# Performance work log

Measured on AMD Instinct MI355X. Metric: run time of the kernel, lower is better.

## Reference

```python
import jax, jax.numpy as jnp
import numpy as np

B, S, D, H = 2, 2048, 1024, 16
HD = D // H  # head depth


def setup_inputs() -> dict:
    key = jax.random.key(0)
    ks = jax.random.split(key, 8)
    scale = 0.02
    K = jax.random.normal(ks[0], (B, S, D), jnp.float32)
    V = jax.random.normal(ks[1], (B, S, D), jnp.float32)
    Q = jax.random.normal(ks[2], (B, S, D), jnp.float32)
    # causal additive mask: 1.0 where attention is disallowed (strict upper triangle)
    mask = jnp.broadcast_to(
        jnp.triu(jnp.ones((S, S), jnp.float32), k=1)[None, None, :, :], (B, 1, S, S)
    )
    Wk = jax.random.normal(ks[3], (D, D), jnp.float32) * scale
    Wv = jax.random.normal(ks[4], (D, D), jnp.float32) * scale
    Wq = jax.random.normal(ks[5], (D, D), jnp.float32) * scale
    Wo = jax.random.normal(ks[6], (D, D), jnp.float32) * scale
    z = jnp.zeros((D,), jnp.float32)
    return {"K": K, "V": V, "Q": Q, "mask": mask,
            "Wk": Wk, "bk": z, "Wv": Wv, "bv": z,
            "Wq": Wq, "bq": z, "Wo": Wo, "bo": z}


def _split_heads(x):  # [B,S,D] -> [B,H,S,HD]
    return x.reshape(B, S, H, HD).transpose(0, 2, 1, 3)


def reference(K, V, Q, mask, Wk, bk, Wv, bv, Wq, bq, Wo, bo):
    k = _split_heads(K @ Wk + bk)
    v = _split_heads(V @ Wv + bv)
    q = _split_heads(Q @ Wq + bq)
    # NOTE: source scales by sqrt(d_model), not sqrt(head_depth)
    logits = jnp.einsum("bhqd,bhkd->bhqk", q, k) / jnp.sqrt(jnp.float32(D))
    logits = logits + mask * (-1e9)
    attn = jax.nn.softmax(logits, axis=-1)
    out = jnp.einsum("bhqk,bhkd->bhqd", attn, v)  # [B,H,S,HD]
    out = out.transpose(0, 2, 1, 3).reshape(B, S, D)
    return out @ Wo + bo
```

## Files before the change

### kernel.cpp

```cpp
#include <hip/hip_runtime.h>
#include <hip/hip_bf16.h>

typedef unsigned short u16;
typedef unsigned int u32;
typedef unsigned long long u64;
typedef __attribute__((ext_vector_type(8))) __bf16 bf16x8;
typedef __attribute__((ext_vector_type(4))) float f32x4;

#define SEQ 2048
#define DM 1024
#define NH 16
#define HDim 64

__device__ __forceinline__ float bf_lo(u32 u) { return __uint_as_float(u << 16); }
__device__ __forceinline__ float bf_hi(u32 u) { return __uint_as_float(u & 0xffff0000u); }
__device__ __forceinline__ u16 f2bf(float f) {
    u32 u = __float_as_uint(f);
    u32 r = (u + 0x7fffu + ((u >> 16) & 1u)) >> 16;
    return (u16)r;
}
__device__ __forceinline__ float bf2f(u16 h) { return __uint_as_float(((u32)h) << 16); }

#define GLD16(g, l)                                                         \
    __builtin_amdgcn_global_load_lds(                                       \
        (const __attribute__((address_space(1))) void*)(g),                 \
        (__attribute__((address_space(3))) void*)(l), 16, 0, 0)

__device__ __forceinline__ bool detect_f32(const u32* q)
{
    const u32 w = q[threadIdx.x & 63];
    const int e0 = ((w & 0xffffu) >> 7) & 0xff;
    const int e1 = (w >> 23) & 0xff;
    const unsigned long long b = __ballot(e0 >= 0x90 || e1 >= 0x90);
    return b != 0ull;
}

__global__ __launch_bounds__(256)
void prep_all(const void* __restrict__ Qin, const void* __restrict__ Kin,
              const void* __restrict__ Vin,
              const void* __restrict__ w0, const void* __restrict__ w1,
              const void* __restrict__ w2, const void* __restrict__ w3,
              const void* __restrict__ b0, const void* __restrict__ b1,
              const void* __restrict__ b2, const void* __restrict__ b3,
              u16* __restrict__ Xall, u16* __restrict__ Wtall,
              u16* __restrict__ ball)
{
    __shared__ u16 T[64 * 66];
    const bool f = detect_f32((const u32*)Qin);
    const int t = threadIdx.x;
    const int bid = blockIdx.x;

    if (bid < 6144) {
        const int z = bid >> 11;
        const int bx = bid & 2047;
        const void* src = (z == 0) ? Qin : (z == 1) ? Kin : Vin;
        const size_t i0 = ((size_t)bx * 256 + t) * 8;
        u16* d = Xall + (size_t)z * 4194304 + i0;
        if (f) {
            const uint4* s = reinterpret_cast<const uint4*>((const float*)src + i0);
            uint4 a = s[0], b = s[1];
            u16 o[8];
            o[0] = f2bf(__uint_as_float(a.x)); o[1] = f2bf(__uint_as_float(a.y));
            o[2] = f2bf(__uint_as_float(a.z)); o[3] = f2bf(__uint_as_float(a.w));
            o[4] = f2bf(__uint_as_float(b.x)); o[5] = f2bf(__uint_as_float(b.y));
            o[6] = f2bf(__uint_as_float(b.z)); o[7] = f2bf(__uint_as_float(b.w));
            *reinterpret_cast<uint4*>(d) = *reinterpret_cast<const uint4*>(o);
        } else {
            *reinterpret_cast<uint4*>(d) =
                *reinterpret_cast<const uint4*>((const u16*)src + i0);
        }
    } else if (bid < 7168) {
        const int r = bid - 6144;
        const int z = r >> 8;
        const void* src = (z == 0) ? w0 : (z == 1) ? w1 : (z == 2) ? w2 : w3;
        const int n0 = ((r >> 4) & 15) * 64;
        const int k0 = (r & 15) * 64;
        const int c = t & 63, g = t >> 6;
        if (f) {
            const float* W = (const float*)src;
#pragma unroll
            for (int i = 0; i < 16; i++) {
                const int kl = g * 16 + i;
                T[kl * 66 + c] = f2bf(W[(size_t)(k0 + kl) * DM + n0 + c]);
            }
        } else {
            const u16* W = (const u16*)src;
#pragma unroll
            for (int i = 0; i < 16; i++) {
                const int kl = g * 16 + i;
                T[kl * 66 + c] = W[(size_t)(k0 + kl) * DM + n0 + c];
            }
        }
        __syncthreads();
        u16* dst = Wtall + (size_t)z * 1048576;
#pragma unroll
        for (int i = 0; i < 16; i++) {
            const int nl = g * 16 + i;
            dst[(size_t)(n0 + nl) * DM + k0 + c] = T[c * 66 + nl];
        }
    } else {
#pragma unroll
        for (int j = 0; j < 16; j++) {
            const int idx = t * 16 + j;
            const int z = idx >> 10, e = idx & 1023;
            const void* src = (z == 0) ? b0 : (z == 1) ? b1 : (z == 2) ? b2 : b3;
            ball[idx] = f ? f2bf(((const float*)src)[e]) : ((const u16*)src)[e];
        }
    }
}

__global__ __launch_bounds__(256)
void gemm128(const u16* __restrict__ Xall, const u16* __restrict__ Wtall,
             const u16* __restrict__ ball, u16* __restrict__ Yall)
{
    __shared__ __align__(16) u16 As[2][128 * 32];
    __shared__ __align__(16) u16 Bs[2][128 * 32];

    const int zz = blockIdx.z;
    const bool swp = (zz != 2);
    const u16* X  = Xall + (size_t)zz * 4194304;
    const u16* Wt = Wtall + (size_t)zz * 1048576;

    const int t    = threadIdx.x;
    const int w    = t >> 6;
    const int lane = t & 63;
    const int quad = lane >> 4;
    const int ln   = lane & 15;
    const int m0   = blockIdx.x * 128;
    const int n0   = blockIdx.y * 128;

    f32x4 acc[4][4];
#pragma unroll
    for (int i = 0; i < 4; i++)
#pragma unroll
        for (int j = 0; j < 4; j++) acc[i][j] = (f32x4){0.f, 0.f, 0.f, 0.f};

    const int swz = (lane >> 3) & 3;
    const u16* ag = X  + (size_t)(m0 + w * 32 + (lane >> 2)) * DM + ((lane & 3) ^ swz) * 8;
    const u16* bg = Wt + (size_t)(n0 + w * 32 + (lane >> 2)) * DM + ((lane & 3) ^ swz) * 8;

    const int wr = (w >> 1) * 64;
    const int wc = (w & 1) * 64;
    const int rs = (quad ^ ((ln >> 1) & 3)) * 8;

#define GSTAGE(B)                                        \
    {                                                    \
        GLD16(ag,           &As[B][w * 1024]);           \
        GLD16(ag + 16 * DM, &As[B][w * 1024 + 512]);     \
        GLD16(bg,           &Bs[B][w * 1024]);           \
        GLD16(bg + 16 * DM, &Bs[B][w * 1024 + 512]);     \
        ag += 32; bg += 32;                              \
    }

#define GCOMP(B)                                                              \
    {                                                                         \
        bf16x8 af[4], bfr[4];                                                 \
        _Pragma("unroll") for (int rt = 0; rt < 4; rt++)                      \
            af[rt] = *reinterpret_cast<const bf16x8*>(                        \
                &As[B][(wr + rt * 16 + ln) * 32 + rs]);                       \
        _Pragma("unroll") for (int ct = 0; ct < 4; ct++)                      \
            bfr[ct] = *reinterpret_cast<const bf16x8*>(                       \
                &Bs[B][(wc + ct * 16 + ln) * 32 + rs]);                       \
        if (swp) {                                                            \
            _Pragma("unroll") for (int rt = 0; rt < 4; rt++)                  \
                _Pragma("unroll") for (int ct = 0; ct < 4; ct++)              \
                    acc[rt][ct] = __builtin_amdgcn_mfma_f32_16x16x32_bf16(    \
                        bfr[ct], af[rt], acc[rt][ct], 0, 0, 0);               \
        } else {                                                              \
            _Pragma("unroll") for (int rt = 0; rt < 4; rt++)                  \
                _Pragma("unroll") for (int ct = 0; ct < 4; ct++)              \
                    acc[rt][ct] = __builtin_amdgcn_mfma_f32_16x16x32_bf16(    \
                        af[rt], bfr[ct], acc[rt][ct], 0, 0, 0);               \
        }                                                                     \
    }

    GSTAGE(0);
    __syncthreads();
#pragma unroll 1
    for (int it = 0; it < 15; ++it) {
        GSTAGE(1); GCOMP(0); __syncthreads();
        GSTAGE(0); GCOMP(1); __syncthreads();
    }
    GSTAGE(1); GCOMP(0); __syncthreads();
    GCOMP(1);
#undef GSTAGE
#undef GCOMP

    u16* Y = Yall + (size_t)zz * 4194304;

    if (swp) {
        const float scale = (zz == 0) ? 0.03125f : 1.0f;
#pragma unroll
        for (int ct = 0; ct < 4; ct++) {
            const int nb = n0 + wc + ct * 16 + quad * 4;
            const int h = nb >> 6, hd = nb & (HDim - 1);
            float bv[4];
#pragma unroll
            for (int r = 0; r < 4; r++) bv[r] = bf2f(ball[zz * 1024 + nb + r]);
#pragma unroll
            for (int rt = 0; rt < 4; rt++) {
                const int m = m0 + wr + rt * 16 + ln;
                const int b = m >> 11, s = m & (SEQ - 1);
                u16 o4[4];
#pragma unroll
                for (int r = 0; r < 4; r++)
                    o4[r] = f2bf((acc[rt][ct][r] + bv[r]) * scale);
                *reinterpret_cast<u64*>(
                    Y + (((size_t)(b * NH + h)) * SEQ + s) * HDim + hd) =
                    *reinterpret_cast<const u64*>(o4);
            }
        }
    } else {
#pragma unroll
        for (int ct = 0; ct < 4; ct++) {
            const int n = n0 + wc + ct * 16 + ln;
            const float bv = bf2f(ball[zz * 1024 + n]);
            const int h = n >> 6, hd = n & (HDim - 1);
#pragma unroll
            for (int rt = 0; rt < 4; rt++) {
                const int m = m0 + wr + rt * 16 + quad * 4;
                const int b = m >> 11, s = m & (SEQ - 1);
                u16 o4[4];
#pragma unroll
                for (int r = 0; r < 4; r++) o4[r] = f2bf(acc[rt][ct][r] + bv);
                *reinterpret_cast<u64*>(
                    Y + (((size_t)(b * NH + h) * HDim + hd) * SEQ + s)) =
                    *reinterpret_cast<const u64*>(o4);
            }
        }
    }
}

__device__ __forceinline__ void attn_tile2(
    const u16* __restrict__ Ks, const u16* __restrict__ Vs,
    u16* __restrict__ Ps, const bf16x8& qf0, const bf16x8& qf1,
    int kt, int qrow, int w, int quad, int ln, f32x4* o, float& l)
{
    f32x4 s[4];
#pragma unroll
    for (int ct = 0; ct < 4; ct++) {
        const u16* kr = &Ks[(ct * 16 + ln) * 72 + quad * 8];
        bf16x8 kf0 = *reinterpret_cast<const bf16x8*>(kr);
        bf16x8 kf1 = *reinterpret_cast<const bf16x8*>(kr + 32);
        f32x4 z = (f32x4){0.f, 0.f, 0.f, 0.f};
        z = __builtin_amdgcn_mfma_f32_16x16x32_bf16(kf0, qf0, z, 0, 0, 0);
        s[ct] = __builtin_amdgcn_mfma_f32_16x16x32_bf16(kf1, qf1, z, 0, 0, 0);
    }
#pragma unroll
    for (int ct = 0; ct < 4; ct++) {
        u16 o4[4];
#pragma unroll
        for (int r = 0; r < 4; r++) {
            const int kcol = kt * 64 + ct * 16 + quad * 4 + r;
            const float e = (kcol <= qrow) ? __expf(s[ct][r]) : 0.f;
            l += e;
            o4[r] = f2bf(e);
        }
        *reinterpret_cast<u64*>(&Ps[(w * 16 + ln) * 72 + ct * 16 + quad * 4]) =
            *reinterpret_cast<const u64*>(o4);
    }
#pragma unroll
    for (int ks = 0; ks < 2; ks++) {
        bf16x8 pf = *reinterpret_cast<const bf16x8*>(
            &Ps[(w * 16 + ln) * 72 + ks * 32 + quad * 8]);
#pragma unroll
        for (int nt = 0; nt < 4; nt++) {
            bf16x8 vf = *reinterpret_cast<const bf16x8*>(
                &Vs[(nt * 16 + ln) * 72 + ks * 32 + quad * 8]);
            o[nt] = __builtin_amdgcn_mfma_f32_16x16x32_bf16(pf, vf, o[nt], 0, 0, 0);
        }
    }
}

__global__ __launch_bounds__(256)
void attn_split(const u16* __restrict__ qh, const u16* __restrict__ kh,
                const u16* __restrict__ vt, u16* __restrict__ Opart,
                float* __restrict__ Lpart)
{
    __shared__ __align__(16) u16 Ks[64 * 72];
    __shared__ __align__(16) u16 Vs[64 * 72];
    __shared__ __align__(16) u16 Ps[64 * 72];

    const int t    = threadIdx.x;
    const int i    = blockIdx.x;
    const int bh   = blockIdx.y;
    const int c    = blockIdx.z;
    const int w    = t >> 6;
    const int lane = t & 63;
    const int quad = lane >> 4;
    const int ln   = lane & 15;
    const int qtH  = 31 - i;
    const int qtL  = i;
    const int m    = (i >= 8) ? 8 : 16 - i;
    const int kt0  = c ? m : 0;
    const int kt1  = c ? (qtH + 1) : m;

    const size_t kbase = (size_t)bh * SEQ * HDim;
    const size_t vbase = (size_t)bh * HDim * SEQ;

    const u16* qrH = qh + kbase + (size_t)(qtH * 64 + w * 16 + ln) * HDim;
    const bf16x8 qfH0 = *reinterpret_cast<const bf16x8*>(qrH + quad * 8);
    const bf16x8 qfH1 = *reinterpret_cast<const bf16x8*>(qrH + 32 + quad * 8);
    const u16* qrL = qh + kbase + (size_t)(qtL * 64 + w * 16 + ln) * HDim;
    const bf16x8 qfL0 = *reinterpret_cast<const bf16x8*>(qrL + quad * 8);
    const bf16x8 qfL1 = *reinterpret_cast<const bf16x8*>(qrL + 32 + quad * 8);

    f32x4 oH[4], oL[4];
    float lH = 0.f, lL = 0.f;
#pragma unroll
    for (int k = 0; k < 4; k++) {
        oH[k] = (f32x4){0.f, 0.f, 0.f, 0.f};
        oL[k] = (f32x4){0.f, 0.f, 0.f, 0.f};
    }

    const int srow = t >> 2;
    const int sc   = (t & 3) * 16;
    const int rowH = qtH * 64 + w * 16 + ln;
    const int rowL = qtL * 64 + w * 16 + ln;

    uint4 kr0, kr1, vr0, vr1;
    {
        const uint4* ksp = reinterpret_cast<const uint4*>(
            kh + kbase + (size_t)(kt0 * 64 + srow) * HDim + sc);
        kr0 = ksp[0]; kr1 = ksp[1];
        const uint4* vsp = reinterpret_cast<const uint4*>(
            vt + vbase + (size_t)srow * SEQ + kt0 * 64 + sc);
        vr0 = vsp[0]; vr1 = vsp[1];
    }

    for (int kt = kt0; kt < kt1; kt++) {
        {
            uint4* kd = reinterpret_cast<uint4*>(&Ks[srow * 72 + sc]);
            kd[0] = kr0; kd[1] = kr1;
            uint4* vd = reinterpret_cast<uint4*>(&Vs[srow * 72 + sc]);
            vd[0] = vr0; vd[1] = vr1;
        }
        __syncthreads();

        if (kt + 1 < kt1) {
            const uint4* ksp = reinterpret_cast<const uint4*>(
                kh + kbase + (size_t)((kt + 1) * 64 + srow) * HDim + sc);
            kr0 = ksp[0]; kr1 = ksp[1];
            const uint4* vsp = reinterpret_cast<const uint4*>(
                vt + vbase + (size_t)srow * SEQ + (kt + 1) * 64 + sc);
            vr0 = vsp[0]; vr1 = vsp[1];
            __builtin_amdgcn_sched_barrier(0);
        }

        attn_tile2(Ks, Vs, Ps, qfH0, qfH1, kt, rowH, w, quad, ln, oH, lH);
        if (kt <= qtL)
            attn_tile2(Ks, Vs, Ps, qfL0, qfL1, kt, rowL, w, quad, ln, oL, lL);

        __syncthreads();
    }

    lH += __shfl_xor(lH, 16); lH += __shfl_xor(lH, 32);
    lL += __shfl_xor(lL, 16); lL += __shfl_xor(lL, 32);

    const size_t cb = ((size_t)c * 32 + bh) * SEQ;
    if (lane < 16) {
        Lpart[cb + qtH * 64 + w * 16 + lane] = lH;
        Lpart[cb + qtL * 64 + w * 16 + lane] = lL;
    }
#pragma unroll
    for (int r = 0; r < 4; r++) {
        const int rH = qtH * 64 + w * 16 + quad * 4 + r;
        const int rL = qtL * 64 + w * 16 + quad * 4 + r;
        u16* dH = Opart + (cb + rH) * HDim + ln;
        u16* dL = Opart + (cb + rL) * HDim + ln;
#pragma unroll
        for (int nt = 0; nt < 4; nt++) {
            dH[nt * 16] = f2bf(oH[nt][r]);
            dL[nt * 16] = f2bf(oL[nt][r]);
        }
    }
}

__global__ __launch_bounds__(256)
void attn_merge(const u16* __restrict__ Opart, const float* __restrict__ Lpart,
                u16* __restrict__ ctx)
{
    const size_t tid8 = (size_t)blockIdx.x * 256 + threadIdx.x;
    const int d8 = (int)(tid8 & 7);
    const int s  = (int)((tid8 >> 3) & (SEQ - 1));
    const int bh = (int)(tid8 >> 14);
    const size_t CSTR = (size_t)32 * SEQ * HDim;

    const uint4 a = *reinterpret_cast<const uint4*>(Opart + tid8 * 8);
    const uint4 b = *reinterpret_cast<const uint4*>(Opart + CSTR + tid8 * 8);
    const float l0 = Lpart[(size_t)bh * SEQ + s];
    const float l1 = Lpart[(size_t)32 * SEQ + (size_t)bh * SEQ + s];
    const float inv = 1.f / (l0 + l1);

    const u32 aw[4] = {a.x, a.y, a.z, a.w};
    const u32 bw[4] = {b.x, b.y, b.z, b.w};
    u32 ow[4];
#pragma unroll
    for (int p = 0; p < 4; p++) {
        const float lo = (bf_lo(aw[p]) + bf_lo(bw[p])) * inv;
        const float hi = (bf_hi(aw[p]) + bf_hi(bw[p])) * inv;
        ow[p] = (u32)f2bf(lo) | ((u32)f2bf(hi) << 16);
    }
    const int bb = bh >> 4, h = bh & 15;
    *reinterpret_cast<uint4*>(
        ctx + ((size_t)(bb * SEQ + s)) * DM + h * HDim + d8 * 8) =
        *reinterpret_cast<const uint4*>(ow);
}

__global__ __launch_bounds__(256)
void gemm_out(const u16* __restrict__ ctx, const u16* __restrict__ Wt,
              const u16* __restrict__ bias, void* __restrict__ dout,
              const u32* __restrict__ qdet)
{
    __shared__ __align__(16) u16 As[2][128 * 32];
    __shared__ __align__(16) u16 Bs[2][64 * 32];

    const int t    = threadIdx.x;
    const int w    = t >> 6;
    const int lane = t & 63;
    const int quad = lane >> 4;
    const int ln   = lane & 15;
    const int m0   = blockIdx.x * 128;
    const int n0   = blockIdx.y * 64;

    f32x4 acc[4][2];
#pragma unroll
    for (int i = 0; i < 4; i++)
#pragma unroll
        for (int j = 0; j < 2; j++) acc[i][j] = (f32x4){0.f, 0.f, 0.f, 0.f};

    const int swz = (lane >> 3) & 3;
    const u16* ag = ctx + (size_t)(m0 + w * 32 + (lane >> 2)) * DM + ((lane & 3) ^ swz) * 8;
    const u16* bg = Wt + (size_t)(n0 + w * 16 + (lane >> 2)) * DM + ((lane & 3) ^ swz) * 8;

    const int wr = (w >> 1) * 64;
    const int wc = (w & 1) * 32;
    const int rs = (quad ^ ((ln >> 1) & 3)) * 8;

#define OSTAGE(B)                                        \
    {                                                    \
        GLD16(ag,           &As[B][w * 1024]);           \
        GLD16(ag + 16 * DM, &As[B][w * 1024 + 512]);     \
        GLD16(bg,           &Bs[B][w * 512]);            \
        ag += 32; bg += 32;                              \
    }

#define OCOMP(B)                                                              \
    {                                                                         \
        bf16x8 af[4], bfr[2];                                                 \
        _Pragma("unroll") for (int rt = 0; rt < 4; rt++)                      \
            af[rt] = *reinterpret_cast<const bf16x8*>(                        \
                &As[B][(wr + rt * 16 + ln) * 32 + rs]);                       \
        _Pragma("unroll") for (int ct = 0; ct < 2; ct++)                      \
            bfr[ct] = *reinterpret_cast<const bf16x8*>(                       \
                &Bs[B][(wc + ct * 16 + ln) * 32 + rs]);                       \
        _Pragma("unroll") for (int rt = 0; rt < 4; rt++)                      \
            _Pragma("unroll") for (int ct = 0; ct < 2; ct++)                  \
                acc[rt][ct] = __builtin_amdgcn_mfma_f32_16x16x32_bf16(        \
                    af[rt], bfr[ct], acc[rt][ct], 0, 0, 0);                   \
    }

    OSTAGE(0);
    __syncthreads();
#pragma unroll 1
    for (int it = 0; it < 15; ++it) {
        OSTAGE(1); OCOMP(0); __syncthreads();
        OSTAGE(0); OCOMP(1); __syncthreads();
    }
    OSTAGE(1); OCOMP(0); __syncthreads();
    OCOMP(1);
#undef OSTAGE
#undef OCOMP

    const bool f = detect_f32(qdet);
#pragma unroll
    for (int ct = 0; ct < 2; ct++) {
        const int n = n0 + wc + ct * 16 + ln;
        const float bv = bf2f(bias[n]);
#pragma unroll
        for (int rt = 0; rt < 4; rt++) {
            const int mb = m0 + wr + rt * 16 + quad * 4;
#pragma unroll
            for (int r = 0; r < 4; r++) {
                const float val = acc[rt][ct][r] + bv;
                if (f) ((float*)dout)[(size_t)(mb + r) * DM + n] = val;
                else   ((u16*)dout)[(size_t)(mb + r) * DM + n] = f2bf(val);
            }
        }
    }
}

__global__ __launch_bounds__(64)
void detect_dtype(const u32* __restrict__ q, int* __restrict__ flag)
{
    const int t = threadIdx.x;
    const u32 w = q[t];
    const int e0 = ((w & 0xffffu) >> 7) & 0xff;
    const int e1 = (w >> 23) & 0xff;
    const unsigned long long b = __ballot(e0 >= 0x90 || e1 >= 0x90);
    if (t == 0) *flag = (b != 0ull) ? 1 : 0;
}

struct AttnAcc { f32x4 o[4]; float l[4]; };

__device__ __forceinline__ void attn_tile(
    const u16* __restrict__ Ks, const u16* __restrict__ Vs,
    u16* __restrict__ Ps, const bf16x8& qf0, const bf16x8& qf1,
    int kt, int rowb, int w, int quad, int ln, AttnAcc& a)
{
    f32x4 s[4];
#pragma unroll
    for (int ct = 0; ct < 4; ct++) {
        const u16* kr = &Ks[(ct * 16 + ln) * 72 + quad * 8];
        bf16x8 kf0 = *reinterpret_cast<const bf16x8*>(kr);
        bf16x8 kf1 = *reinterpret_cast<const bf16x8*>(kr + 32);
        f32x4 z = (f32x4){0.f, 0.f, 0.f, 0.f};
        z = __builtin_amdgcn_mfma_f32_16x16x32_bf16(qf0, kf0, z, 0, 0, 0);
        s[ct] = __builtin_amdgcn_mfma_f32_16x16x32_bf16(qf1, kf1, z, 0, 0, 0);
    }
#pragma unroll
    for (int ct = 0; ct < 4; ct++) {
        const int kcol = kt * 64 + ct * 16 + ln;
#pragma unroll
        for (int r = 0; r < 4; r++) {
            const float e = (kcol <= rowb + r) ? __expf(s[ct][r]) : 0.f;
            a.l[r] += e;
            Ps[(w * 16 + quad * 4 + r) * 68 + ct * 16 + ln] = f2bf(e);
        }
    }
#pragma unroll
    for (int ks = 0; ks < 2; ks++) {
        bf16x8 pf = *reinterpret_cast<const bf16x8*>(
            &Ps[(w * 16 + ln) * 68 + ks * 32 + quad * 8]);
#pragma unroll
        for (int nt = 0; nt < 4; nt++) {
            bf16x8 vf = *reinterpret_cast<const bf16x8*>(
                &Vs[(nt * 16 + ln) * 72 + ks * 32 + quad * 8]);
            a.o[nt] = __builtin_amdgcn_mfma_f32_16x16x32_bf16(pf, vf, a.o[nt], 0, 0, 0);
        }
    }
}

__global__ __launch_bounds__(256)
void attn_mfma(const u16* __restrict__ qh, const u16* __restrict__ kh,
               const u16* __restrict__ vt, u16* __restrict__ ctx)
{
    __shared__ __align__(16) u16 Ks[64 * 72];
    __shared__ __align__(16) u16 Vs[64 * 72];
    __shared__ __align__(16) u16 Ps[64 * 68];

    const int t    = threadIdx.x;
    const int i    = blockIdx.x;
    const int bh   = blockIdx.y;
    const int w    = t >> 6;
    const int lane = t & 63;
    const int quad = lane >> 4;
    const int ln   = lane & 15;
    const int qtH  = 31 - i;
    const int qtL  = i;

    const size_t kbase = (size_t)bh * SEQ * HDim;
    const size_t vbase = (size_t)bh * HDim * SEQ;

    const u16* qrH = qh + kbase + (size_t)(qtH * 64 + w * 16 + ln) * HDim;
    const bf16x8 qfH0 = *reinterpret_cast<const bf16x8*>(qrH + quad * 8);
    const bf16x8 qfH1 = *reinterpret_cast<const bf16x8*>(qrH + 32 + quad * 8);
    const u16* qrL = qh + kbase + (size_t)(qtL * 64 + w * 16 + ln) * HDim;
    const bf16x8 qfL0 = *reinterpret_cast<const bf16x8*>(qrL + quad * 8);
    const bf16x8 qfL1 = *reinterpret_cast<const bf16x8*>(qrL + 32 + quad * 8);

    AttnAcc aH, aL;
#pragma unroll
    for (int k = 0; k < 4; k++) {
        aH.o[k] = (f32x4){0.f, 0.f, 0.f, 0.f}; aH.l[k] = 0.f;
        aL.o[k] = (f32x4){0.f, 0.f, 0.f, 0.f}; aL.l[k] = 0.f;
    }

    const int srow = t >> 2;
    const int sc   = (t & 3) * 16;
    const int rowHb = qtH * 64 + w * 16 + quad * 4;
    const int rowLb = qtL * 64 + w * 16 + quad * 4;

    for (int kt = 0; kt <= qtH; kt++) {
        {
            const uint4* ks = reinterpret_cast<const uint4*>(
                kh + kbase + (size_t)(kt * 64 + srow) * HDim + sc);
            uint4* kd = reinterpret_cast<uint4*>(&Ks[srow * 72 + sc]);
            kd[0] = ks[0];
            kd[1] = ks[1];
            const uint4* vs = reinterpret_cast<const uint4*>(
                vt + vbase + (size_t)srow * SEQ + kt * 64 + sc);
            uint4* vd = reinterpret_cast<uint4*>(&Vs[srow * 72 + sc]);
            vd[0] = vs[0];
            vd[1] = vs[1];
        }
        __syncthreads();

        attn_tile(Ks, Vs, Ps, qfH0, qfH1, kt, rowHb, w, quad, ln, aH);
        if (kt <= qtL)
            attn_tile(Ks, Vs, Ps, qfL0, qfL1, kt, rowLb, w, quad, ln, aL);

        __syncthreads();
    }

#pragma unroll
    for (int m = 1; m < 16; m <<= 1) {
#pragma unroll
        for (int r = 0; r < 4; r++) {
            aH.l[r] += __shfl_xor(aH.l[r], m);
            aL.l[r] += __shfl_xor(aL.l[r], m);
        }
    }

    const int b = bh >> 4;
    const int h = bh & 15;
#pragma unroll
    for (int r = 0; r < 4; r++) {
        const float invH = 1.f / aH.l[r];
        const float invL = 1.f / aL.l[r];
        const int sH = qtH * 64 + w * 16 + quad * 4 + r;
        const int sL = qtL * 64 + w * 16 + quad * 4 + r;
        u16* dH = ctx + ((size_t)(b * SEQ + sH)) * DM + h * HDim + ln;
        u16* dL = ctx + ((size_t)(b * SEQ + sL)) * DM + h * HDim + ln;
#pragma unroll
        for (int nt = 0; nt < 4; nt++) {
            dH[nt * 16] = f2bf(aH.o[nt][r] * invH);
            dL[nt * 16] = f2bf(aL.o[nt][r] * invL);
        }
    }
}

__global__ __launch_bounds__(256)
void gemm_bias(const void* __restrict__ Xv, const void* __restrict__ Wv,
               const void* __restrict__ biasv, void* __restrict__ Yv,
               int M, int N, int K, int mode, int xsel, int wsel, int ysel,
               float scale, const int* __restrict__ flagp)
{
    __shared__ __align__(16) u16 As[64 * 32];
    __shared__ __align__(16) u16 Bs[64 * 40];

    const int f  = *flagp;
    const bool xf = (xsel != 0) && (f != 0);
    const bool wf = (wsel != 0) && (f != 0);
    const bool yf = (ysel != 0) && (f != 0);

    const u16*   Xb = (const u16*)Xv;
    const float* Xf = (const float*)Xv;
    const u16*   Wb = (const u16*)Wv;
    const float* Wf = (const float*)Wv;

    const int t    = threadIdx.x;
    const int m0   = blockIdx.y * 64;
    const int n0   = blockIdx.x * 64;
    const int w    = t >> 6;
    const int lane = t & 63;
    const int quad = lane >> 4;
    const int ln   = lane & 15;

    f32x4 acc[4];
#pragma unroll
    for (int i = 0; i < 4; i++) acc[i] = (f32x4){0.f, 0.f, 0.f, 0.f};

    const int a_row = t >> 2;
    const int a_c8  = (t & 3) * 8;
    const int b_n   = t & 63;
    const int b_k8  = (t >> 6) * 8;

    for (int kk = 0; kk < K; kk += 32) {
        const size_t aoff = (size_t)(m0 + a_row) * K + kk + a_c8;
        if (!xf) {
            *reinterpret_cast<uint4*>(&As[a_row * 32 + a_c8]) =
                *reinterpret_cast<const uint4*>(Xb + aoff);
        } else {
            const float* src = Xf + aoff;
            uint4 u0 = reinterpret_cast<const uint4*>(src)[0];
            uint4 u1 = reinterpret_cast<const uint4*>(src)[1];
            u16 tmp[8];
            tmp[0] = f2bf(__uint_as_float(u0.x));
            tmp[1] = f2bf(__uint_as_float(u0.y));
            tmp[2] = f2bf(__uint_as_float(u0.z));
            tmp[3] = f2bf(__uint_as_float(u0.w));
            tmp[4] = f2bf(__uint_as_float(u1.x));
            tmp[5] = f2bf(__uint_as_float(u1.y));
            tmp[6] = f2bf(__uint_as_float(u1.z));
            tmp[7] = f2bf(__uint_as_float(u1.w));
            *reinterpret_cast<uint4*>(&As[a_row * 32 + a_c8]) =
                *reinterpret_cast<const uint4*>(tmp);
        }
        u16 tmp[8];
        if (!wf) {
#pragma unroll
            for (int j = 0; j < 8; j++)
                tmp[j] = Wb[(size_t)(kk + b_k8 + j) * N + n0 + b_n];
        } else {
#pragma unroll
            for (int j = 0; j < 8; j++)
                tmp[j] = f2bf(Wf[(size_t)(kk + b_k8 + j) * N + n0 + b_n]);
        }
        *reinterpret_cast<uint4*>(&Bs[b_n * 40 + b_k8]) =
            *reinterpret_cast<const uint4*>(tmp);

        __syncthreads();

        bf16x8 bfrag = *reinterpret_cast<const bf16x8*>(&Bs[(w * 16 + ln) * 40 + quad * 8]);
#pragma unroll
        for (int rt = 0; rt < 4; rt++) {
            bf16x8 afrag = *reinterpret_cast<const bf16x8*>(&As[(rt * 16 + ln) * 32 + quad * 8]);
            acc[rt] = __builtin_amdgcn_mfma_f32_16x16x32_bf16(afrag, bfrag, acc[rt], 0, 0, 0);
        }
        __syncthreads();
    }

    const int n = n0 + w * 16 + ln;
    const float bv = wf ? ((const float*)biasv)[n] : bf2f(((const u16*)biasv)[n]);
#pragma unroll
    for (int rt = 0; rt < 4; rt++) {
        if (mode == 2) {
            const int m = m0 + rt * 16 + quad * 4;
            const int b = m >> 11;
            const int s = m & (SEQ - 1);
            const int h = n >> 6;
            const int hd = n & (HDim - 1);
            u16 o4[4];
#pragma unroll
            for (int r = 0; r < 4; r++) o4[r] = f2bf((acc[rt][r] + bv) * scale);
            *reinterpret_cast<u64*>(
                (u16*)Yv + (((size_t)(b * NH + h) * HDim + hd) * SEQ + s)) =
                *reinterpret_cast<const u64*>(o4);
        } else {
#pragma unroll
            for (int r = 0; r < 4; r++) {
                const int m = m0 + rt * 16 + quad * 4 + r;
                const float val = (acc[rt][r] + bv) * scale;
                if (mode == 0) {
                    if (yf) ((float*)Yv)[(size_t)m * N + n] = val;
                    else    ((u16*)Yv)[(size_t)m * N + n] = f2bf(val);
                } else {
                    const int b = m >> 11;
                    const int s = m & (SEQ - 1);
                    const int h = n >> 6;
                    const int hd = n & (HDim - 1);
                    ((u16*)Yv)[(((size_t)(b * NH + h)) * SEQ + s) * HDim + hd] = f2bf(val);
                }
            }
        }
    }
}

extern "C" void kernel_launch(void* const* d_in, const int* in_sizes, int n_in,
                              void* d_out, int out_size, void* d_ws, size_t ws_size,
                              hipStream_t stream)
{
    const void* Kin = d_in[0];
    const void* Vin = d_in[1];
    const void* Qin = d_in[2];
    const void* Wk = d_in[4];
    const void* bk = d_in[5];
    const void* Wv = d_in[6];
    const void* bv = d_in[7];
    const void* Wq = d_in[8];
    const void* bq = d_in[9];
    const void* Wo = d_in[10];
    const void* bo = d_in[11];

    char* ws = (char*)d_ws;
    const size_t NEED = ((size_t)29360128 + 4096) * 2 + 256;

    if (ws_size >= NEED) {
        u16* Xall  = (u16*)ws;
        u16* Yall  = (u16*)ws + 12582912;
        u16* Wtall = (u16*)ws + 25165824;
        u16* ball  = (u16*)ws + 29360128;
        u16* qhp   = Yall;
        u16* khp   = Yall + 4194304;
        u16* vtp   = Yall + 8388608;
        u16* ctx   = Xall;
        u16* Opart = Xall + 4194304;
        float* Lpart = (float*)Wtall;

        hipLaunchKernelGGL(prep_all, dim3(7169), dim3(256), 0, stream,
                           Qin, Kin, Vin, Wq, Wk, Wv, Wo, bq, bk, bv, bo,
                           Xall, Wtall, ball);

        hipLaunchKernelGGL(gemm128, dim3(32, 8, 3), dim3(256), 0, stream,
                           Xall, Wtall, ball, Yall);

        hipLaunchKernelGGL(attn_split, dim3(16, 32, 2), dim3(256), 0, stream,
                           qhp, khp, vtp, Opart, Lpart);

        hipLaunchKernelGGL(attn_merge, dim3(2048), dim3(256), 0, stream,
                           Opart, Lpart, ctx);

        hipLaunchKernelGGL(gemm_out, dim3(32, 16), dim3(256), 0, stream,
                           ctx, Wtall + (size_t)3 * 1048576, ball + 3 * 1024,
                           d_out, (const u32*)Qin);
    } else {
        const size_t SEG = (size_t)2 * SEQ * DM * sizeof(u16);
        u16* qh  = (u16*)(ws);
        u16* khd = (u16*)(ws + SEG);
        u16* vtd = (u16*)(ws + 2 * SEG);
        u16* ctx = (u16*)(ws + 3 * SEG);
        int* flag = (int*)(ws + 4 * SEG);

        hipLaunchKernelGGL(detect_dtype, dim3(1), dim3(64), 0, stream,
                           (const u32*)Qin, flag);

        const int M = 2 * SEQ;
        dim3 ggrid(DM / 64, M / 64);
        dim3 gblk(256);

        hipLaunchKernelGGL(gemm_bias, ggrid, gblk, 0, stream, Qin, Wq, bq, qh,  M, DM, DM, 1, 1, 1, 0, 0.03125f, flag);
        hipLaunchKernelGGL(gemm_bias, ggrid, gblk, 0, stream, Kin, Wk, bk, khd, M, DM, DM, 1, 1, 1, 0, 1.0f,     flag);
        hipLaunchKernelGGL(gemm_bias, ggrid, gblk, 0, stream, Vin, Wv, bv, vtd, M, DM, DM, 2, 1, 1, 0, 1.0f,     flag);

        hipLaunchKernelGGL(attn_mfma, dim3(16, 2 * NH), dim3(256), 0,
                           stream, qh, khd, vtd, ctx);

        hipLaunchKernelGGL(gemm_bias, ggrid, gblk, 0, stream, ctx, Wo, bo, d_out, M, DM, DM, 0, 0, 1, 1, 1.0f, flag);
    }
}
```

Baseline: 258.5 us.

## Use partial vmcnt waits with raw barriers, MFMA priority, and XCD-aware attention block mapping

Replaces __syncthreads in the projection and output GEMM double-buffer loops with explicit s_waitcnt vmcnt(N) plus s_barrier. This lets the next stage's global-to-LDS loads stay in flight while the current buffer is computed, instead of draining every outstanding load. It also raises wave priority around the MFMA sections of the attention tile. Attention blocks are remapped so that all blocks for one batch-head land on the same XCD, for better L2 reuse of K and V. The hand-tuned vmcnt counts must match the number of loads each stage issues, or the GEMMs could read stale LDS data.

```diff
diff --git a/kernel.cpp b/kernel.cpp
--- a/kernel.cpp
+++ b/kernel.cpp
@@ -25,6 +25,10 @@
     __builtin_amdgcn_global_load_lds(                                       \
         (const __attribute__((address_space(1))) void*)(g),                 \
         (__attribute__((address_space(3))) void*)(l), 16, 0, 0)
+
+#define VWAIT_BAR(N)                                                        \
+    asm volatile("s_waitcnt vmcnt(" #N ")\n\ts_barrier" ::: "memory")
+#define BAR_ONLY()  asm volatile("s_barrier" ::: "memory")
 
 __device__ __forceinline__ bool detect_f32(const u32* q)
 {
@@ -175,13 +179,23 @@
     }
 
     GSTAGE(0);
-    __syncthreads();
 #pragma unroll 1
     for (int it = 0; it < 15; ++it) {
-        GSTAGE(1); GCOMP(0); __syncthreads();
-        GSTAGE(0); GCOMP(1); __syncthreads();
-    }
-    GSTAGE(1); GCOMP(0); __syncthreads();
+        GSTAGE(1);
+        VWAIT_BAR(4);
+        GCOMP(0);
+        BAR_ONLY();
+        GSTAGE(0);
+        VWAIT_BAR(4);
+        GCOMP(1);
+        BAR_ONLY();
+    }
+    GSTAGE(1);
+    VWAIT_BAR(4);
+    GCOMP(0);
+    BAR_ONLY();
+    asm volatile("s_waitcnt vmcnt(0)" ::: "memory");
+    __builtin_amdgcn_s_barrier();
     GCOMP(1);
 #undef GSTAGE
 #undef GCOMP
@@ -237,6 +251,7 @@
     int kt, int qrow, int w, int quad, int ln, f32x4* o, float& l)
 {
     f32x4 s[4];
+    __builtin_amdgcn_s_setprio(1);
 #pragma unroll
     for (int ct = 0; ct < 4; ct++) {
         const u16* kr = &Ks[(ct * 16 + ln) * 72 + quad * 8];
@@ -246,6 +261,7 @@
         z = __builtin_amdgcn_mfma_f32_16x16x32_bf16(kf0, qf0, z, 0, 0, 0);
         s[ct] = __builtin_amdgcn_mfma_f32_16x16x32_bf16(kf1, qf1, z, 0, 0, 0);
     }
+    __builtin_amdgcn_s_setprio(0);
 #pragma unroll
     for (int ct = 0; ct < 4; ct++) {
         u16 o4[4];
@@ -259,6 +275,7 @@
         *reinterpret_cast<u64*>(&Ps[(w * 16 + ln) * 72 + ct * 16 + quad * 4]) =
             *reinterpret_cast<const u64*>(o4);
     }
+    __builtin_amdgcn_s_setprio(1);
 #pragma unroll
     for (int ks = 0; ks < 2; ks++) {
         bf16x8 pf = *reinterpret_cast<const bf16x8*>(
@@ -270,6 +287,7 @@
             o[nt] = __builtin_amdgcn_mfma_f32_16x16x32_bf16(pf, vf, o[nt], 0, 0, 0);
         }
     }
+    __builtin_amdgcn_s_setprio(0);
 }
 
 __global__ __launch_bounds__(256)
@@ -282,9 +300,14 @@
     __shared__ __align__(16) u16 Ps[64 * 72];
 
     const int t    = threadIdx.x;
-    const int i    = blockIdx.x;
-    const int bh   = blockIdx.y;
-    const int c    = blockIdx.z;
+    const int L    = blockIdx.x + 16 * (blockIdx.y + 32 * blockIdx.z);
+    const int xcd  = L & 7;
+    const int slot = L >> 3;
+    const int bh   = xcd + 8 * (slot >> 5);
+    const int rr   = slot & 31;
+    const int i    = rr & 15;
+    const int c    = rr >> 4;
+
     const int w    = t >> 6;
     const int lane = t & 63;
     const int quad = lane >> 4;
@@ -461,13 +484,23 @@
     }
 
     OSTAGE(0);
-    __syncthreads();
 #pragma unroll 1
     for (int it = 0; it < 15; ++it) {
-        OSTAGE(1); OCOMP(0); __syncthreads();
-        OSTAGE(0); OCOMP(1); __syncthreads();
-    }
-    OSTAGE(1); OCOMP(0); __syncthreads();
+        OSTAGE(1);
+        VWAIT_BAR(3);
+        OCOMP(0);
+        BAR_ONLY();
+        OSTAGE(0);
+        VWAIT_BAR(3);
+        OCOMP(1);
+        BAR_ONLY();
+    }
+    OSTAGE(1);
+    VWAIT_BAR(3);
+    OCOMP(0);
+    BAR_ONLY();
+    asm volatile("s_waitcnt vmcnt(0)" ::: "memory");
+    __builtin_amdgcn_s_barrier();
     OCOMP(1);
 #undef OSTAGE
 #undef OCOMP
```

Result: no change. 258.1 us (-0.2%).
